# Kernel optimization log

Hardware: AMD Instinct MI355X
Metric: run time of the kernel (lower is better)

Reference implementation:

```python
import jax, jax.numpy as jnp
import numpy as np

EMBED_DIM = 1024
NUM_HEADS = 16
HEAD_DIM = EMBED_DIM // NUM_HEADS


def setup_inputs() -> dict:
    key = jax.random.key(0)
    ks = jax.random.split(key, 10)
    B, T, E = 2, 2048, EMBED_DIM

    def xavier(k, shape):
        fan_in, fan_out = shape[1], shape[0]
        limit = (6.0 / (fan_in + fan_out)) ** 0.5
        return jax.random.uniform(k, shape, jnp.float32, -limit, limit)

    return {
        "query": jax.random.normal(ks[0], (B, T, E), jnp.float32),
        "key": jax.random.normal(ks[1], (B, T, E), jnp.float32),
        "value": jax.random.normal(ks[2], (B, T, E), jnp.float32),
        "Wq": xavier(ks[3], (E, E)),
        "Wk": xavier(ks[4], (E, E)),
        "Wv": xavier(ks[5], (E, E)),
        "bq": jnp.zeros((E,), jnp.float32),
        "bk": jnp.zeros((E,), jnp.float32),
        "bv": jnp.zeros((E,), jnp.float32),
        "Wo": xavier(ks[6], (E, E)),
        "bo": jnp.zeros((E,), jnp.float32),
    }


def reference(query, key, value, Wq, Wk, Wv, bq, bk, bv, Wo, bo):
    B, Tq, E = query.shape
    Tk = key.shape[1]
    H, hd = NUM_HEADS, HEAD_DIM

    # In-projections (nn.Linear convention: x @ W.T + b)
    q = query @ Wq.T + bq  # (B, Tq, E)
    k = key @ Wk.T + bk    # (B, Tk, E)
    v = value @ Wv.T + bv  # (B, Tk, E)

    # Split heads -> (B, H, T, hd)
    q = q.reshape(B, Tq, H, hd).transpose(0, 2, 1, 3)
    k = k.reshape(B, Tk, H, hd).transpose(0, 2, 1, 3)
    v = v.reshape(B, Tk, H, hd).transpose(0, 2, 1, 3)

    # Scaled dot-product attention (dropout=0, no mask)
    scores = jnp.einsum("bhqd,bhkd->bhqk", q, k) / jnp.sqrt(jnp.float32(hd))
    attn = jax.nn.softmax(scores, axis=-1)
    out = jnp.einsum("bhqk,bhkd->bhqd", attn, v)  # (B, H, Tq, hd)

    # Merge heads and out-projection
    out = out.transpose(0, 2, 1, 3).reshape(B, Tq, E)
    return out @ Wo.T + bo
```

## Files before the change

### kernel.cpp

```cpp
#include <hip/hip_runtime.h>
#include <hip/hip_bf16.h>
#include <stdint.h>


#define NHEAD 16
#define SEQT  2048
#define EDIM  1024
#define HD    64
#define MB    2
#define MTOT  (MB*SEQT)

typedef __attribute__((ext_vector_type(4)))  float f32x4;
typedef __attribute__((ext_vector_type(16))) float f32x16;
typedef __attribute__((ext_vector_type(8)))  short s16x8;

typedef const __attribute__((address_space(1))) void* GPtr;
typedef __attribute__((address_space(3))) void* LPtr;

static __device__ __forceinline__ ushort f2bf(float f) {
    uint32_t u = __float_as_uint(f);
    u += 0x7FFF + ((u >> 16) & 1);
    return (ushort)(u >> 16);
}
static __device__ __forceinline__ float bf2f(ushort h) {
    return __uint_as_float(((uint32_t)h) << 16);
}
static __device__ __forceinline__ void gload_lds16(const void* g, void* l) {
    __builtin_amdgcn_global_load_lds((GPtr)g, (LPtr)l, 16, 0, 0);
}
static __device__ __forceinline__ uint cvt_pk_bf16(float lo, float hi) {
    uint r;
    asm("v_cvt_pk_bf16_f32 %0, %1, %2" : "=v"(r) : "v"(lo), "v"(hi));
    return r;
}

__global__ void cvt_kernel(const float* __restrict__ src, ushort* __restrict__ dst, int n4) {
    int idx = blockIdx.x * blockDim.x + threadIdx.x;
    int stride = gridDim.x * blockDim.x;
    for (int i = idx; i < n4; i += stride) {
        float4 v = reinterpret_cast<const float4*>(src)[i];
        ushort4 o;
        o.x = f2bf(v.x); o.y = f2bf(v.y); o.z = f2bf(v.z); o.w = f2bf(v.w);
        reinterpret_cast<ushort4*>(dst)[i] = o;
    }
}

template<int OUTMODE>
__device__ __forceinline__ void gemm_body(const ushort* __restrict__ A,
                                          const ushort* __restrict__ W,
                                          const float* __restrict__ bias,
                                          void* __restrict__ out)
{
    const int K = 1024, N = 1024;
    __shared__ ushort As[128 * 32];
    __shared__ ushort Bs[128 * 32];

    const int tid  = threadIdx.x;
    const int lane = tid & 63;
    const int wid  = tid >> 6;
    const int wr = wid >> 1, wc = wid & 1;
    const int bm = blockIdx.y, bn = blockIdx.x;

    f32x4 acc[4][4];
#pragma unroll
    for (int i = 0; i < 4; i++)
#pragma unroll
        for (int j = 0; j < 4; j++) acc[i][j] = (f32x4){0.f, 0.f, 0.f, 0.f};

    const ushort* Abase = A + (size_t)(bm * 128) * K;
    const ushort* Wbase = W + (size_t)(bn * 128) * K;
    ushort* AsW = As + wid * 512;
    ushort* BsW = Bs + wid * 512;
    const int srow = tid >> 2;
    const int scol = (tid & 3) * 8;

    const int afoff = (wr * 64 + (lane & 15)) * 32 + (lane >> 4) * 8;
    const int bfoff = (wc * 64 + (lane & 15)) * 32 + (lane >> 4) * 8;

    for (int k0 = 0; k0 < K; k0 += 32) {
#pragma unroll
        for (int j = 0; j < 2; j++) {
            gload_lds16(Abase + (size_t)(j * 64 + srow) * K + k0 + scol, AsW + j * 2048);
            gload_lds16(Wbase + (size_t)(j * 64 + srow) * K + k0 + scol, BsW + j * 2048);
        }
        __syncthreads();

        s16x8 af[4], bf[4];
#pragma unroll
        for (int i = 0; i < 4; i++)
            af[i] = *reinterpret_cast<const s16x8*>(&As[afoff + i * 16 * 32]);
#pragma unroll
        for (int j = 0; j < 4; j++)
            bf[j] = *reinterpret_cast<const s16x8*>(&Bs[bfoff + j * 16 * 32]);
#pragma unroll
        for (int i = 0; i < 4; i++)
#pragma unroll
            for (int j = 0; j < 4; j++)
                acc[i][j] = __builtin_amdgcn_mfma_f32_16x16x32_bf16(af[i], bf[j], acc[i][j], 0, 0, 0);
        __syncthreads();
    }

    const int orow0 = bm * 128 + wr * 64 + (lane >> 4) * 4;
    const int ocol0 = bn * 128 + wc * 64 + (lane & 15);
#pragma unroll
    for (int i = 0; i < 4; i++) {
#pragma unroll
        for (int j = 0; j < 4; j++) {
            int col = ocol0 + j * 16;
#pragma unroll
            for (int r = 0; r < 4; r++) {
                int row = orow0 + i * 16 + r;
                float bv = (OUTMODE == 2) ? bias[row] : bias[col];
                float v = acc[i][j][r] + bv;
                if (OUTMODE == 0) {
                    int b = row >> 11, t = row & (SEQT - 1);
                    int h = col >> 6,  d = col & 63;
                    ((ushort*)out)[(((size_t)b * NHEAD + h) * SEQT + t) * HD + d] = f2bf(v);
                } else if (OUTMODE == 1) {
                    ((float*)out)[(size_t)row * N + col] = v;
                } else if (OUTMODE == 2) {
                    int h = row >> 6, d = row & 63;
                    int b = col >> 11, t = col & (SEQT - 1);
                    int tsw = (t & ~63) | ((t & 63) ^ ((d & 7) << 3));
                    ((ushort*)out)[(((size_t)b * NHEAD + h) * HD + d) * SEQT + tsw] = f2bf(v);
                } else {
                    int b = row >> 11, t = row & (SEQT - 1);
                    int h = col >> 6,  d = col & 63;
                    int dsw = d ^ ((t & 7) << 3);
                    ((ushort*)out)[(((size_t)b * NHEAD + h) * SEQT + t) * HD + dsw] = f2bf(v);
                }
            }
        }
    }
}

__global__ __launch_bounds__(256, 2)
void projQ_kernel(const ushort* A, const ushort* W, const float* bi, ushort* o) {
    gemm_body<0>(A, W, bi, o);
}
__global__ __launch_bounds__(256, 2)
void projK_kernel(const ushort* A, const ushort* W, const float* bi, ushort* o) {
    gemm_body<3>(A, W, bi, o);
}
__global__ __launch_bounds__(256, 2)
void projVT_kernel(const ushort* A, const ushort* W, const float* bi, ushort* o) {
    gemm_body<2>(A, W, bi, o);
}
__global__ __launch_bounds__(256, 2)
void oproj_kernel(const ushort* __restrict__ A, const ushort* __restrict__ W,
                  const float* __restrict__ bias, float* __restrict__ out) {
    gemm_body<1>(A, W, bias, out);
}

#define KBLK 64
#define NT (SEQT / KBLK)

__global__ __launch_bounds__(256)
void attn_kernel(const ushort* __restrict__ Qg, const ushort* __restrict__ Kg,
                 const ushort* __restrict__ Vtg, ushort* __restrict__ Og)
{
    __shared__ ushort Ks[2][KBLK * HD];
    __shared__ ushort Vs[2][HD * KBLK];

    const int tid  = threadIdx.x;
    const int lane = tid & 63;
    const int wid  = tid >> 6;
    const int g    = lane >> 5;
    const int qc   = lane & 31;
    const int bh   = blockIdx.y;
    const int q0   = blockIdx.x * 128 + wid * 32;

    const ushort* Kp = Kg  + (size_t)bh * SEQT * HD;
    const ushort* Vp = Vtg + (size_t)bh * HD * SEQT;

    const float CS = 0.18033688011112042f;
    s16x8 qf[4];
    {
        const ushort* Qp = Qg + ((size_t)bh * SEQT + q0 + qc) * HD;
#pragma unroll
        for (int kst = 0; kst < 4; kst++) {
            s16x8 raw = *reinterpret_cast<const s16x8*>(Qp + kst * 16 + g * 8);
            s16x8 sc;
#pragma unroll
            for (int j = 0; j < 8; j++) sc[j] = (short)f2bf(bf2f((ushort)raw[j]) * CS);
            qf[kst] = sc;
        }
    }

    f32x16 oa[2];
#pragma unroll
    for (int mt = 0; mt < 2; mt++)
#pragma unroll
        for (int r = 0; r < 16; r++) oa[mt][r] = 0.f;
    float mrow = -1e30f, lrow = 0.f;

#define STAGE(buf, t0)                                                               \
    do {                                                                             \
        _Pragma("unroll")                                                            \
        for (int c = 0; c < 2; c++) {                                                \
            int i = c * 256 + tid;                                                   \
            gload_lds16(Kp + (size_t)((t0) + (i >> 3)) * HD + (i & 7) * 8,           \
                        &Ks[buf][(c * 256 + wid * 64) * 8]);                         \
            gload_lds16(Vp + (size_t)(i >> 3) * SEQT + (t0) + (i & 7) * 8,           \
                        &Vs[buf][(c * 256 + wid * 64) * 8]);                         \
        }                                                                            \
    } while (0)

    STAGE(0, 0);
    __syncthreads();
    int cur = 0;

    for (int t = 0; t < NT; t++) {
        if (t + 1 < NT) STAGE(cur ^ 1, (t + 1) * KBLK);
        const ushort* Kb = Ks[cur];
        const ushort* Vb = Vs[cur];

        f32x16 sa[2];
#pragma unroll
        for (int mt = 0; mt < 2; mt++) {
            f32x16 a;
#pragma unroll
            for (int r = 0; r < 16; r++) a[r] = 0.f;
            const int key = mt * 32 + qc;
#pragma unroll
            for (int kst = 0; kst < 4; kst++) {
                int dsw = (kst * 16 + g * 8) ^ ((key & 7) << 3);
                s16x8 kf = *reinterpret_cast<const s16x8*>(Kb + key * HD + dsw);
                a = __builtin_amdgcn_mfma_f32_32x32x16_bf16(kf, qf[kst], a, 0, 0, 0);
            }
            sa[mt] = a;
        }

        float mx = sa[0][0];
#pragma unroll
        for (int r = 1; r < 16; r++) mx = fmaxf(mx, sa[0][r]);
#pragma unroll
        for (int r = 0; r < 16; r++) mx = fmaxf(mx, sa[1][r]);
        mx = fmaxf(mx, __shfl_xor(mx, 32));
        float mn = fmaxf(mrow, mx);
        float alpha = exp2f(mrow - mn);
        mrow = mn;
        float rs = 0.f;
#pragma unroll
        for (int mt = 0; mt < 2; mt++)
#pragma unroll
            for (int r = 0; r < 16; r++) {
                float p = exp2f(sa[mt][r] - mn);
                sa[mt][r] = p;
                rs += p;
            }
        rs += __shfl_xor(rs, 32);
        lrow = lrow * alpha + rs;
#pragma unroll
        for (int mt = 0; mt < 2; mt++)
#pragma unroll
            for (int r = 0; r < 16; r++) oa[mt][r] *= alpha;

        uint pk[2][8];
#pragma unroll
        for (int aa = 0; aa < 2; aa++)
#pragma unroll
            for (int p = 0; p < 8; p++)
                pk[aa][p] = cvt_pk_bf16(sa[aa][2 * p], sa[aa][2 * p + 1]);

#pragma unroll
        for (int kst = 0; kst < 4; kst++) {
            const int aa = kst >> 1;
            const int b4 = (kst & 1) * 4;
            uint s0 = g ? pk[aa][b4 + 0] : pk[aa][b4 + 2];
            uint s1 = g ? pk[aa][b4 + 1] : pk[aa][b4 + 3];
            uint r0 = __shfl_xor(s0, 32);
            uint r1 = __shfl_xor(s1, 32);
            union { uint u[4]; s16x8 v; } pf;
            pf.u[0] = g ? r0 : pk[aa][b4 + 0];
            pf.u[1] = g ? r1 : pk[aa][b4 + 1];
            pf.u[2] = g ? pk[aa][b4 + 2] : r0;
            pf.u[3] = g ? pk[aa][b4 + 3] : r1;
#pragma unroll
            for (int mt = 0; mt < 2; mt++) {
                const int d = mt * 32 + qc;
                int ksw = (kst * 16 + g * 8) ^ ((d & 7) << 3);
                s16x8 vf = *reinterpret_cast<const s16x8*>(Vb + d * KBLK + ksw);
                oa[mt] = __builtin_amdgcn_mfma_f32_32x32x16_bf16(vf, pf.v, oa[mt], 0, 0, 0);
            }
        }
        __syncthreads();
        cur ^= 1;
    }

    float inv = 1.0f / lrow;
    ushort* Ob = &Ks[0][0] + wid * 2048;
#pragma unroll
    for (int mt = 0; mt < 2; mt++)
#pragma unroll
        for (int p = 0; p < 8; p++) {
            int d = mt * 32 + ((2 * p) & 3) + 8 * (p >> 1) + 4 * g;
            uint v = cvt_pk_bf16(oa[mt][2 * p] * inv, oa[mt][2 * p + 1] * inv);
            *reinterpret_cast<uint*>(Ob + qc * HD + (d ^ ((qc & 7) << 3))) = v;
        }
    __syncthreads();
    const int b = bh >> 4, h = bh & 15;
    const int qr = lane >> 1, dh = (lane & 1) * 32;
    ushort* dst = Og + ((size_t)b * SEQT + q0 + qr) * EDIM + h * HD + dh;
    const ushort* src = Ob + qr * HD;
#pragma unroll
    for (int c = 0; c < 4; c++) {
        int d0 = (dh + c * 8) ^ ((qr & 7) << 3);
        *reinterpret_cast<s16x8*>(dst + c * 8) = *reinterpret_cast<const s16x8*>(src + d0);
    }
}

extern "C" void kernel_launch(void* const* d_in, const int* in_sizes, int n_in,
                              void* d_out, int out_size, void* d_ws, size_t ws_size,
                              hipStream_t stream)
{
    const float* query = (const float*)d_in[0];
    const float* key   = (const float*)d_in[1];
    const float* value = (const float*)d_in[2];
    const float* Wq    = (const float*)d_in[3];
    const float* Wk    = (const float*)d_in[4];
    const float* Wv    = (const float*)d_in[5];
    const float* bq    = (const float*)d_in[6];
    const float* bk    = (const float*)d_in[7];
    const float* bv    = (const float*)d_in[8];
    const float* Wo    = (const float*)d_in[9];
    const float* bo    = (const float*)d_in[10];
    float* out = (float*)d_out;

    const size_t NX = (size_t)MTOT * EDIM;
    const size_t NW = (size_t)EDIM * EDIM;
    ushort* ws = (ushort*)d_ws;
    ushort* xq  = ws;
    ushort* xk  = xq + NX;
    ushort* xv  = xk + NX;
    ushort* wq  = xv + NX;
    ushort* wk  = wq + NW;
    ushort* wv  = wk + NW;
    ushort* wo  = wv + NW;
    ushort* qb  = wo + NW;
    ushort* kb  = qb + NX;
    ushort* vtb = kb + NX;
    ushort* ao  = vtb + NX;

    const int n4x = (int)(NX / 4), n4w = (int)(NW / 4);
    cvt_kernel<<<dim3(1024), 256, 0, stream>>>(query, xq, n4x);
    cvt_kernel<<<dim3(1024), 256, 0, stream>>>(key,   xk, n4x);
    cvt_kernel<<<dim3(1024), 256, 0, stream>>>(value, xv, n4x);
    cvt_kernel<<<dim3(512),  256, 0, stream>>>(Wq, wq, n4w);
    cvt_kernel<<<dim3(512),  256, 0, stream>>>(Wk, wk, n4w);
    cvt_kernel<<<dim3(512),  256, 0, stream>>>(Wv, wv, n4w);
    cvt_kernel<<<dim3(512),  256, 0, stream>>>(Wo, wo, n4w);

    projQ_kernel <<<dim3(8, 32),  256, 0, stream>>>(xq, wq, bq, qb);
    projK_kernel <<<dim3(8, 32),  256, 0, stream>>>(xk, wk, bk, kb);
    projVT_kernel<<<dim3(32, 8),  256, 0, stream>>>(wv, xv, bv, vtb);

    attn_kernel<<<dim3(SEQT / 128, MB * NHEAD), 256, 0, stream>>>(qb, kb, vtb, ao);

    oproj_kernel<<<dim3(8, 32), 256, 0, stream>>>(ao, wo, bo, out);
}
```

Measured before the change: 298.6 us.

## Batch conversion and projection launches, triple-buffer attention, lazy softmax rescale

Merges the seven fp32-to-bf16 conversions into one launch and the three input projections into one z-indexed launch, so each wave of work fills the GPU at once. The attention kernel moves from double to triple buffering of K/V tiles, using explicit vmcnt waits and raw barriers so loads run two tiles ahead. It raises wave priority around the MFMA blocks. It also skips the output rescale when the running max grows by no more than a threshold. This adds LDS use and relies on careful manual wait counts.

```diff
diff --git a/kernel.cpp b/kernel.cpp
--- a/kernel.cpp
+++ b/kernel.cpp
@@ -34,14 +34,31 @@
     return r;
 }
 
-__global__ void cvt_kernel(const float* __restrict__ src, ushort* __restrict__ dst, int n4) {
+#define N4X ((MTOT * EDIM) / 4)
+#define N4W ((EDIM * EDIM) / 4)
+
+__global__ void cvt_batch(const float* q, const float* k, const float* v,
+                          const float* Wq, const float* Wk, const float* Wv,
+                          const float* Wo,
+                          ushort* xq, ushort* xk, ushort* xv,
+                          ushort* wq, ushort* wk, ushort* wv, ushort* wo)
+{
+    int z = blockIdx.z;
+    const float* s; ushort* d; int n4;
+    if      (z == 0) { s = q;  d = xq; n4 = N4X; }
+    else if (z == 1) { s = k;  d = xk; n4 = N4X; }
+    else if (z == 2) { s = v;  d = xv; n4 = N4X; }
+    else if (z == 3) { s = Wq; d = wq; n4 = N4W; }
+    else if (z == 4) { s = Wk; d = wk; n4 = N4W; }
+    else if (z == 5) { s = Wv; d = wv; n4 = N4W; }
+    else             { s = Wo; d = wo; n4 = N4W; }
     int idx = blockIdx.x * blockDim.x + threadIdx.x;
     int stride = gridDim.x * blockDim.x;
     for (int i = idx; i < n4; i += stride) {
-        float4 v = reinterpret_cast<const float4*>(src)[i];
+        float4 vv = reinterpret_cast<const float4*>(s)[i];
         ushort4 o;
-        o.x = f2bf(v.x); o.y = f2bf(v.y); o.z = f2bf(v.z); o.w = f2bf(v.w);
-        reinterpret_cast<ushort4*>(dst)[i] = o;
+        o.x = f2bf(vv.x); o.y = f2bf(vv.y); o.z = f2bf(vv.z); o.w = f2bf(vv.w);
+        reinterpret_cast<ushort4*>(d)[i] = o;
     }
 }
 
@@ -49,7 +66,8 @@
 __device__ __forceinline__ void gemm_body(const ushort* __restrict__ A,
                                           const ushort* __restrict__ W,
                                           const float* __restrict__ bias,
-                                          void* __restrict__ out)
+                                          void* __restrict__ out,
+                                          int bm, int bn)
 {
     const int K = 1024, N = 1024;
     __shared__ ushort As[128 * 32];
@@ -59,7 +77,6 @@
     const int lane = tid & 63;
     const int wid  = tid >> 6;
     const int wr = wid >> 1, wc = wid & 1;
-    const int bm = blockIdx.y, bn = blockIdx.x;
 
     f32x4 acc[4][4];
 #pragma unroll
@@ -135,21 +152,22 @@
 }
 
 __global__ __launch_bounds__(256, 2)
-void projQ_kernel(const ushort* A, const ushort* W, const float* bi, ushort* o) {
-    gemm_body<0>(A, W, bi, o);
-}
-__global__ __launch_bounds__(256, 2)
-void projK_kernel(const ushort* A, const ushort* W, const float* bi, ushort* o) {
-    gemm_body<3>(A, W, bi, o);
-}
-__global__ __launch_bounds__(256, 2)
-void projVT_kernel(const ushort* A, const ushort* W, const float* bi, ushort* o) {
-    gemm_body<2>(A, W, bi, o);
-}
+void proj3_kernel(const ushort* xq, const ushort* xk, const ushort* xv,
+                  const ushort* wq, const ushort* wk, const ushort* wv,
+                  const float* bq, const float* bk, const float* bv,
+                  ushort* oq, ushort* ok, ushort* ov)
+{
+    int z = blockIdx.z;
+    if (z == 0)      gemm_body<0>(xq, wq, bq, oq, blockIdx.x, blockIdx.y);
+    else if (z == 1) gemm_body<3>(xk, wk, bk, ok, blockIdx.x, blockIdx.y);
+    else             gemm_body<2>(wv, xv, bv, ov, blockIdx.y, blockIdx.x);
+}
+
 __global__ __launch_bounds__(256, 2)
 void oproj_kernel(const ushort* __restrict__ A, const ushort* __restrict__ W,
-                  const float* __restrict__ bias, float* __restrict__ out) {
-    gemm_body<1>(A, W, bias, out);
+                  const float* __restrict__ bias, float* __restrict__ out)
+{
+    gemm_body<1>(A, W, bias, out, blockIdx.y, blockIdx.x);
 }
 
 #define KBLK 64
@@ -159,8 +177,8 @@
 void attn_kernel(const ushort* __restrict__ Qg, const ushort* __restrict__ Kg,
                  const ushort* __restrict__ Vtg, ushort* __restrict__ Og)
 {
-    __shared__ ushort Ks[2][KBLK * HD];
-    __shared__ ushort Vs[2][HD * KBLK];
+    __shared__ ushort Ks[3][KBLK * HD];
+    __shared__ ushort Vs[3][HD * KBLK];
 
     const int tid  = threadIdx.x;
     const int lane = tid & 63;
@@ -207,15 +225,17 @@
     } while (0)
 
     STAGE(0, 0);
-    __syncthreads();
-    int cur = 0;
+    STAGE(1, KBLK);
+    asm volatile("s_waitcnt vmcnt(4)" ::: "memory");
+    __builtin_amdgcn_s_barrier();
 
     for (int t = 0; t < NT; t++) {
-        if (t + 1 < NT) STAGE(cur ^ 1, (t + 1) * KBLK);
-        const ushort* Kb = Ks[cur];
-        const ushort* Vb = Vs[cur];
+        if (t + 2 < NT) STAGE((t + 2) % 3, (t + 2) * KBLK);
+        const ushort* Kb = Ks[t % 3];
+        const ushort* Vb = Vs[t % 3];
 
         f32x16 sa[2];
+        __builtin_amdgcn_s_setprio(1);
 #pragma unroll
         for (int mt = 0; mt < 2; mt++) {
             f32x16 a;
@@ -230,6 +250,7 @@
             }
             sa[mt] = a;
         }
+        __builtin_amdgcn_s_setprio(0);
 
         float mx = sa[0][0];
 #pragma unroll
@@ -237,24 +258,27 @@
 #pragma unroll
         for (int r = 0; r < 16; r++) mx = fmaxf(mx, sa[1][r]);
         mx = fmaxf(mx, __shfl_xor(mx, 32));
-        float mn = fmaxf(mrow, mx);
-        float alpha = exp2f(mrow - mn);
-        mrow = mn;
+        if (!__all(mx <= mrow + 4.0f)) {
+            float mn = fmaxf(mrow, mx);
+            float alpha = exp2f(mrow - mn);
+            mrow = mn;
+            lrow *= alpha;
+#pragma unroll
+            for (int mt = 0; mt < 2; mt++)
+#pragma unroll
+                for (int r = 0; r < 16; r++) oa[mt][r] *= alpha;
+        }
         float rs = 0.f;
 #pragma unroll
         for (int mt = 0; mt < 2; mt++)
 #pragma unroll
             for (int r = 0; r < 16; r++) {
-                float p = exp2f(sa[mt][r] - mn);
+                float p = exp2f(sa[mt][r] - mrow);
                 sa[mt][r] = p;
                 rs += p;
             }
         rs += __shfl_xor(rs, 32);
-        lrow = lrow * alpha + rs;
-#pragma unroll
-        for (int mt = 0; mt < 2; mt++)
-#pragma unroll
-            for (int r = 0; r < 16; r++) oa[mt][r] *= alpha;
+        lrow += rs;
 
         uint pk[2][8];
 #pragma unroll
@@ -276,6 +300,7 @@
             pf.u[1] = g ? r1 : pk[aa][b4 + 1];
             pf.u[2] = g ? pk[aa][b4 + 2] : r0;
             pf.u[3] = g ? pk[aa][b4 + 3] : r1;
+            __builtin_amdgcn_s_setprio(1);
 #pragma unroll
             for (int mt = 0; mt < 2; mt++) {
                 const int d = mt * 32 + qc;
@@ -283,9 +308,12 @@
                 s16x8 vf = *reinterpret_cast<const s16x8*>(Vb + d * KBLK + ksw);
                 oa[mt] = __builtin_amdgcn_mfma_f32_32x32x16_bf16(vf, pf.v, oa[mt], 0, 0, 0);
             }
-        }
-        __syncthreads();
-        cur ^= 1;
+            __builtin_amdgcn_s_setprio(0);
+        }
+
+        if (t + 2 < NT)       asm volatile("s_waitcnt vmcnt(4)" ::: "memory");
+        else if (t + 2 == NT) asm volatile("s_waitcnt vmcnt(0)" ::: "memory");
+        __builtin_amdgcn_s_barrier();
     }
 
     float inv = 1.0f / lrow;
@@ -342,18 +370,11 @@
     ushort* vtb = kb + NX;
     ushort* ao  = vtb + NX;
 
-    const int n4x = (int)(NX / 4), n4w = (int)(NW / 4);
-    cvt_kernel<<<dim3(1024), 256, 0, stream>>>(query, xq, n4x);
-    cvt_kernel<<<dim3(1024), 256, 0, stream>>>(key,   xk, n4x);
-    cvt_kernel<<<dim3(1024), 256, 0, stream>>>(value, xv, n4x);
-    cvt_kernel<<<dim3(512),  256, 0, stream>>>(Wq, wq, n4w);
-    cvt_kernel<<<dim3(512),  256, 0, stream>>>(Wk, wk, n4w);
-    cvt_kernel<<<dim3(512),  256, 0, stream>>>(Wv, wv, n4w);
-    cvt_kernel<<<dim3(512),  256, 0, stream>>>(Wo, wo, n4w);
-
-    projQ_kernel <<<dim3(8, 32),  256, 0, stream>>>(xq, wq, bq, qb);
-    projK_kernel <<<dim3(8, 32),  256, 0, stream>>>(xk, wk, bk, kb);
-    projVT_kernel<<<dim3(32, 8),  256, 0, stream>>>(wv, xv, bv, vtb);
+    cvt_batch<<<dim3(128, 1, 7), 256, 0, stream>>>(query, key, value, Wq, Wk, Wv, Wo,
+                                                   xq, xk, xv, wq, wk, wv, wo);
+
+    proj3_kernel<<<dim3(32, 8, 3), 256, 0, stream>>>(xq, xk, xv, wq, wk, wv,
+                                                     bq, bk, bv, qb, kb, vtb);
 
     attn_kernel<<<dim3(SEQT / 128, MB * NHEAD), 256, 0, stream>>>(qb, kb, vtb, ao);
 
```

Result: faster. 269.0 us (-9.9%).
